# Performance work log

Measured on AMD Instinct MI355X. Metric: run time of the kernel, lower is better.

Reference implementation:

```python
import jax, jax.numpy as jnp
import numpy as np

B, F, D = 4096, 39, 16
L0, L1 = 128, 128
H1 = L0 // 2  # split_half: half the maps feed the next layer


def setup_inputs() -> dict:
    key = jax.random.key(0)
    k0, k1, k2, k3, k4 = jax.random.split(key, 5)
    x = jax.random.normal(k0, (B, F, D), dtype=jnp.float32)
    # Conv1D(size, 1, channels_first) == matmul over channel dim: W [out, in]
    W0 = jax.random.normal(k1, (L0, F * F), dtype=jnp.float32) * 0.02
    b0 = jnp.zeros((L0,), dtype=jnp.float32)
    W1 = jax.random.normal(k2, (L1, H1 * F), dtype=jnp.float32) * 0.02
    b1 = jnp.zeros((L1,), dtype=jnp.float32)
    return {"x": x, "W0": W0, "b0": b0, "W1": W1, "b1": b1}


def _cin_layer(h, h0, W, b):
    # h: [B, H, D], h0: [B, F, D] -> outer product [B, H*F, D], then 1x1 conv
    z = jnp.einsum('bhd,bmd->bhmd', h, h0)
    z = z.reshape(z.shape[0], -1, z.shape[-1])          # [B, H*F, D]
    y = jnp.einsum('oc,bcd->bod', W, z) + b[None, :, None]
    return jax.nn.relu(y)


def reference(x, W0, b0, W1, b1):
    h0 = x
    # layer 0 (split_half, not last): split into next_hidden / direct_connect
    y0 = _cin_layer(h0, h0, W0, b0)                     # [B, L0, D]
    next_hidden, direct0 = y0[:, :H1, :], y0[:, H1:, :]
    # layer 1 (last): all maps are direct connect
    direct1 = _cin_layer(next_hidden, h0, W1, b1)       # [B, L1, D]
    result = jnp.sum(jnp.concatenate([direct0, direct1], axis=1), axis=-1)
    return result  # [B, L0//2 + L1]
```

## Files before the change

kernel.cpp:

```cpp
#include <hip/hip_runtime.h>
#include <hip/hip_fp16.h>

#define B_     4096
#define F_     39
#define NKK    130
#define KKPAD  132
#define PFD    2
#define WPANEL ((size_t)KKPAD * 128)

typedef _Float16 f16x8  __attribute__((ext_vector_type(8)));
typedef float    f32x4  __attribute__((ext_vector_type(4)));
typedef float    f32x16 __attribute__((ext_vector_type(16)));

union FragAB { f16x8 h8; __half2 h2[4]; f32x4 f4; unsigned u[4]; __half h[8]; };

__global__ __launch_bounds__(256) void prep_w(
    const float* __restrict__ W0, const float* __restrict__ W1,
    __half* __restrict__ Wp)
{
    int idx = blockIdx.x * 256 + threadIdx.x;
    if (idx >= 4 * 130 * 1024) return;
    int j    = idx & 7;
    int lane = (idx >> 3) & 63;
    int ks   = (idx >> 9) & 1;
    int rest = idx >> 10;
    int kk   = rest % 130, Mt = rest / 130;
    int o    = Mt * 32 + (lane & 31);
    int sub  = lane >> 5;
    float v = 0.f;
    if (kk < 50) {
        int seg = kk / 10, kkin = kk - seg * 10;
        int h = 4 * kkin + 2 * ks + sub;
        int m = seg * 8 + j;
        if (h < 39 && m < 39) v = W0[o * 1521 + h * 39 + m];
    } else {
        int l = kk - 50;
        int seg = l / 10, kkin = l - seg * 10;
        int m = 4 * kkin + 2 * ks + sub;
        int h = seg * 8 + j;
        if (m < 39) v = W1[o * 2496 + h * 39 + m];
    }
    Wp[((size_t)(Mt * KKPAD + kk) * 2 + ks) * 512 + lane * 8 + j] = __float2half(v);
}

__global__ __launch_bounds__(256, 2) void cin_main(
    const float* __restrict__ x, const float* __restrict__ b0,
    const float* __restrict__ b1, const __half* __restrict__ Wp,
    float* __restrict__ out)
{
    __shared__ __align__(16) __half xT[8][16][40];
    __shared__ __align__(16) __half nhT[8][16][68];
    __shared__ float bs0[128], bs1[128];

    const int t    = threadIdx.x;
    const int w    = t >> 6, lane = t & 63;
    const int sub  = lane >> 5, bp = (lane >> 4) & 1, d = lane & 15;
    const int gb   = blockIdx.x * 8;

    const f32x4* Ap = (const f32x4*)Wp + (size_t)w * WPANEL + lane;
    FragAB An[PFD][2];
#pragma unroll
    for (int i = 0; i < PFD; ++i) {
        An[i][0].f4 = Ap[(size_t)i * 128];
        An[i][1].f4 = Ap[(size_t)i * 128 + 64];
    }

    if (t < 128) { bs0[t] = b0[t]; bs1[t] = b1[t]; }

    for (int i = t; i < 1248; i += 256) {
        int bt = i / 156, r2 = i - bt * 156;
        int f = r2 >> 2, dq = r2 & 3;
        float4 v = *(const float4*)&x[((size_t)(gb + bt) * F_ + f) * 16 + dq * 4];
        xT[bt][dq * 4 + 0][f] = __float2half(v.x);
        xT[bt][dq * 4 + 1][f] = __float2half(v.y);
        xT[bt][dq * 4 + 2][f] = __float2half(v.z);
        xT[bt][dq * 4 + 3][f] = __float2half(v.w);
    }
    if (t < 128) xT[t >> 4][t & 15][39] = __float2half(0.f);
    __syncthreads();

    FragAB xmc[4][5];
#pragma unroll
    for (int p = 0; p < 4; ++p)
#pragma unroll
        for (int a = 0; a < 5; ++a)
            xmc[p][a].f4 = *(const f32x4*)&xT[2 * p + bp][d][a * 8];

    const unsigned psel = sub ? 0x03020302u : 0x01000100u;

    f32x16 acc[4];
#pragma unroll
    for (int r = 0; r < 16; ++r) {
        float bv = bs0[w * 32 + (r & 3) + 8 * (r >> 2) + 4 * sub];
#pragma unroll
        for (int p = 0; p < 4; ++p) acc[p][r] = bv;
    }

    int kk = 0;
#pragma unroll 1
    for (int seg = 0; seg < 13; ++seg) {
        if (seg == 5) {
            if (w < 2) {
#pragma unroll
                for (int p = 0; p < 4; ++p) {
                    __half* nr = &nhT[2 * p + bp][d][0];
#pragma unroll
                    for (int rq = 0; rq < 4; ++rq) {
                        union { __half h[4]; float2 f2; } pk;
#pragma unroll
                        for (int q = 0; q < 4; ++q)
                            pk.h[q] = __float2half(fmaxf(acc[p][rq * 4 + q], 0.f));
                        *(float2*)(nr + w * 32 + 8 * rq + 4 * sub) = pk.f2;
                    }
                }
            } else {
#pragma unroll
                for (int p = 0; p < 4; ++p) {
#pragma unroll
                    for (int rq = 0; rq < 4; ++rq) {
                        float4 s; float* sv = (float*)&s;
#pragma unroll
                        for (int q = 0; q < 4; ++q) {
                            float v = fmaxf(acc[p][rq * 4 + q], 0.f);
                            v += __shfl_xor(v, 1); v += __shfl_xor(v, 2);
                            v += __shfl_xor(v, 4); v += __shfl_xor(v, 8);
                            sv[q] = v;
                        }
                        if (d == 0) {
                            int row = w * 32 + 8 * rq + 4 * sub;
                            *(float4*)&out[(size_t)(gb + 2 * p + bp) * 192 + (row - 64)] = s;
                        }
                    }
                }
            }
#pragma unroll
            for (int r = 0; r < 16; ++r) {
                float bv = bs1[w * 32 + (r & 3) + 8 * (r >> 2) + 4 * sub];
#pragma unroll
                for (int p = 0; p < 4; ++p) acc[p][r] = bv;
            }
            __syncthreads();
        }

        FragAB xcur[4];
        if (seg < 5) {
#pragma unroll
            for (int p = 0; p < 4; ++p)
                xcur[p].f4 = *(const f32x4*)&xT[2 * p + bp][d][seg * 8];
        } else {
#pragma unroll
            for (int p = 0; p < 4; ++p)
                xcur[p].f4 = *(const f32x4*)&nhT[2 * p + bp][d][(seg - 5) * 8];
        }

#pragma unroll
        for (int kkin = 0; kkin < 10; ++kkin) {
            const int s = kkin & 1;

            __builtin_amdgcn_s_setprio(1);
#pragma unroll
            for (int ks = 0; ks < 2; ++ks) {
                const int ee = 2 * kkin + ks;
#pragma unroll
                for (int p = 0; p < 4; ++p) {
                    unsigned bc = __builtin_amdgcn_perm(0u, xmc[p][ee >> 2].u[ee & 3], psel);
                    __half2 xh2 = *(__half2*)&bc;
                    FragAB bfr;
#pragma unroll
                    for (int q = 0; q < 4; ++q)
                        bfr.h2[q] = __hmul2(xcur[p].h2[q], xh2);
                    acc[p] = __builtin_amdgcn_mfma_f32_32x32x16_f16(
                        An[s][ks].h8, bfr.h8, acc[p], 0, 0, 0);
                }
            }
            __builtin_amdgcn_s_setprio(0);

            An[s][0].f4 = Ap[(size_t)(kk + PFD) * 128];
            An[s][1].f4 = Ap[(size_t)(kk + PFD) * 128 + 64];
            ++kk;
        }
    }

#pragma unroll
    for (int p = 0; p < 4; ++p) {
#pragma unroll
        for (int rq = 0; rq < 4; ++rq) {
            float4 s; float* sv = (float*)&s;
#pragma unroll
            for (int q = 0; q < 4; ++q) {
                float v = fmaxf(acc[p][rq * 4 + q], 0.f);
                v += __shfl_xor(v, 1); v += __shfl_xor(v, 2);
                v += __shfl_xor(v, 4); v += __shfl_xor(v, 8);
                sv[q] = v;
            }
            if (d == 0) {
                int row = w * 32 + 8 * rq + 4 * sub;
                *(float4*)&out[(size_t)(gb + 2 * p + bp) * 192 + 64 + row] = s;
            }
        }
    }
}

extern "C" void kernel_launch(void* const* d_in, const int* in_sizes, int n_in,
                              void* d_out, int out_size, void* d_ws, size_t ws_size,
                              hipStream_t stream) {
    const float* x  = (const float*)d_in[0];
    const float* W0 = (const float*)d_in[1];
    const float* b0 = (const float*)d_in[2];
    const float* W1 = (const float*)d_in[3];
    const float* b1 = (const float*)d_in[4];
    float* out = (float*)d_out;
    __half* Wp = (__half*)d_ws;

    prep_w<<<(4 * 130 * 1024 + 255) / 256, 256, 0, stream>>>(W0, W1, Wp);
    cin_main<<<B_ / 8, 256, 0, stream>>>(x, b0, b1, Wp, out);
}
```

Measured before the change: 74.12 us.

## Fully unroll segment loop with five-deep double-buffered weight fragment prefetch

Replaces the runtime segment loop with compile-time unrolled segment bodies that load weight A-fragments in batches of five k-steps into two register banks, alternating them so global loads overlap MFMA work. Layer-0 segments now read the x column straight from the resident xmc registers instead of reloading xT from LDS. The nhT row padding goes from 68 to 72 and the s_setprio hints are dropped. This trades many more VGPRs (20 fragment registers live) and larger code for deeper latency hiding, which risks spills or lower occupancy under the two-blocks-per-CU launch bound.

Measured after the change: 76.55 us. +3.3%, slower.

```diff
diff --git a/kernel.cpp b/kernel.cpp
--- a/kernel.cpp
+++ b/kernel.cpp
@@ -3,9 +3,7 @@
 
 #define B_     4096
 #define F_     39
-#define NKK    130
 #define KKPAD  132
-#define PFD    2
 #define WPANEL ((size_t)KKPAD * 128)
 
 typedef _Float16 f16x8  __attribute__((ext_vector_type(8)));
@@ -43,13 +41,66 @@
     Wp[((size_t)(Mt * KKPAD + kk) * 2 + ks) * 512 + lane * 8 + j] = __float2half(v);
 }
 
+template<int LL, int AA, int EB>
+__device__ __forceinline__ void compute_half(
+    const FragAB (&Areg)[5][2], const FragAB (&xmc)[4][5],
+    const FragAB (&xcur)[4], f32x16 (&acc)[4], unsigned psel)
+{
+#pragma unroll
+    for (int i = 0; i < 5; ++i) {
+#pragma unroll
+        for (int ks = 0; ks < 2; ++ks) {
+            const int ee = EB + 2 * i + ks;
+#pragma unroll
+            for (int p = 0; p < 4; ++p) {
+                unsigned bc = __builtin_amdgcn_perm(0u, xmc[p][ee >> 2].u[ee & 3], psel);
+                __half2 xh2 = *(__half2*)&bc;
+                FragAB bfr;
+#pragma unroll
+                for (int q = 0; q < 4; ++q) {
+                    if constexpr (LL == 0)
+                        bfr.h2[q] = __hmul2(xmc[p][AA].h2[q], xh2);
+                    else
+                        bfr.h2[q] = __hmul2(xcur[p].h2[q], xh2);
+                }
+                acc[p] = __builtin_amdgcn_mfma_f32_32x32x16_f16(
+                    Areg[i][ks].h8, bfr.h8, acc[p], 0, 0, 0);
+            }
+        }
+    }
+}
+
+template<int LL, int AA, bool LAST>
+__device__ __forceinline__ void seg_body(
+    const f32x4*& Apos,
+    FragAB (&Aa)[5][2], FragAB (&Ab)[5][2],
+    const FragAB (&xmc)[4][5], const FragAB (&xcur)[4],
+    f32x16 (&acc)[4], unsigned psel)
+{
+#pragma unroll
+    for (int i = 0; i < 5; ++i) {
+        Ab[i][0].f4 = Apos[(5 + i) * 128];
+        Ab[i][1].f4 = Apos[(5 + i) * 128 + 64];
+    }
+    compute_half<LL, AA, 0>(Aa, xmc, xcur, acc, psel);
+    if (!LAST) {
+#pragma unroll
+        for (int i = 0; i < 5; ++i) {
+            Aa[i][0].f4 = Apos[(10 + i) * 128];
+            Aa[i][1].f4 = Apos[(10 + i) * 128 + 64];
+        }
+    }
+    compute_half<LL, AA, 10>(Ab, xmc, xcur, acc, psel);
+    Apos += 1280;
+}
+
 __global__ __launch_bounds__(256, 2) void cin_main(
     const float* __restrict__ x, const float* __restrict__ b0,
     const float* __restrict__ b1, const __half* __restrict__ Wp,
     float* __restrict__ out)
 {
     __shared__ __align__(16) __half xT[8][16][40];
-    __shared__ __align__(16) __half nhT[8][16][68];
+    __shared__ __align__(16) __half nhT[8][16][72];
     __shared__ float bs0[128], bs1[128];
 
     const int t    = threadIdx.x;
@@ -57,12 +108,12 @@
     const int sub  = lane >> 5, bp = (lane >> 4) & 1, d = lane & 15;
     const int gb   = blockIdx.x * 8;
 
-    const f32x4* Ap = (const f32x4*)Wp + (size_t)w * WPANEL + lane;
-    FragAB An[PFD][2];
-#pragma unroll
-    for (int i = 0; i < PFD; ++i) {
-        An[i][0].f4 = Ap[(size_t)i * 128];
-        An[i][1].f4 = Ap[(size_t)i * 128 + 64];
+    const f32x4* Apos = (const f32x4*)Wp + (size_t)w * WPANEL + lane;
+    FragAB Aa[5][2], Ab[5][2];
+#pragma unroll
+    for (int i = 0; i < 5; ++i) {
+        Aa[i][0].f4 = Apos[i * 128];
+        Aa[i][1].f4 = Apos[i * 128 + 64];
     }
 
     if (t < 128) { bs0[t] = b0[t]; bs1[t] = b1[t]; }
@@ -96,90 +147,71 @@
         for (int p = 0; p < 4; ++p) acc[p][r] = bv;
     }
 
-    int kk = 0;
-#pragma unroll 1
-    for (int seg = 0; seg < 13; ++seg) {
-        if (seg == 5) {
-            if (w < 2) {
-#pragma unroll
-                for (int p = 0; p < 4; ++p) {
-                    __half* nr = &nhT[2 * p + bp][d][0];
-#pragma unroll
-                    for (int rq = 0; rq < 4; ++rq) {
-                        union { __half h[4]; float2 f2; } pk;
-#pragma unroll
-                        for (int q = 0; q < 4; ++q)
-                            pk.h[q] = __float2half(fmaxf(acc[p][rq * 4 + q], 0.f));
-                        *(float2*)(nr + w * 32 + 8 * rq + 4 * sub) = pk.f2;
-                    }
+    FragAB xcur[4];
+
+    seg_body<0, 0, false>(Apos, Aa, Ab, xmc, xcur, acc, psel);
+    seg_body<0, 1, false>(Apos, Aa, Ab, xmc, xcur, acc, psel);
+    seg_body<0, 2, false>(Apos, Aa, Ab, xmc, xcur, acc, psel);
+    seg_body<0, 3, false>(Apos, Aa, Ab, xmc, xcur, acc, psel);
+    seg_body<0, 4, false>(Apos, Aa, Ab, xmc, xcur, acc, psel);
+
+    if (w < 2) {
+#pragma unroll
+        for (int p = 0; p < 4; ++p) {
+            __half* nr = &nhT[2 * p + bp][d][0];
+#pragma unroll
+            for (int rq = 0; rq < 4; ++rq) {
+                union { __half h[4]; float2 f2; } pk;
+#pragma unroll
+                for (int q = 0; q < 4; ++q)
+                    pk.h[q] = __float2half(fmaxf(acc[p][rq * 4 + q], 0.f));
+                *(float2*)(nr + w * 32 + 8 * rq + 4 * sub) = pk.f2;
+            }
+        }
+    } else {
+#pragma unroll
+        for (int p = 0; p < 4; ++p) {
+#pragma unroll
+            for (int rq = 0; rq < 4; ++rq) {
+                float4 s; float* sv = (float*)&s;
+#pragma unroll
+                for (int q = 0; q < 4; ++q) {
+                    float v = fmaxf(acc[p][rq * 4 + q], 0.f);
+                    v += __shfl_xor(v, 1); v += __shfl_xor(v, 2);
+                    v += __shfl_xor(v, 4); v += __shfl_xor(v, 8);
+                    sv[q] = v;
                 }
-            } else {
-#pragma unroll
-                for (int p = 0; p < 4; ++p) {
-#pragma unroll
-                    for (int rq = 0; rq < 4; ++rq) {
-                        float4 s; float* sv = (float*)&s;
-#pragma unroll
-                        for (int q = 0; q < 4; ++q) {
-                            float v = fmaxf(acc[p][rq * 4 + q], 0.f);
-                            v += __shfl_xor(v, 1); v += __shfl_xor(v, 2);
-                            v += __shfl_xor(v, 4); v += __shfl_xor(v, 8);
-                            sv[q] = v;
-                        }
-                        if (d == 0) {
-                            int row = w * 32 + 8 * rq + 4 * sub;
-                            *(float4*)&out[(size_t)(gb + 2 * p + bp) * 192 + (row - 64)] = s;
-                        }
-                    }
+                if (d == 0) {
+                    int row = w * 32 + 8 * rq + 4 * sub;
+                    *(float4*)&out[(size_t)(gb + 2 * p + bp) * 192 + (row - 64)] = s;
                 }
             }
-#pragma unroll
-            for (int r = 0; r < 16; ++r) {
-                float bv = bs1[w * 32 + (r & 3) + 8 * (r >> 2) + 4 * sub];
-#pragma unroll
-                for (int p = 0; p < 4; ++p) acc[p][r] = bv;
-            }
-            __syncthreads();
-        }
-
-        FragAB xcur[4];
-        if (seg < 5) {
-#pragma unroll
-            for (int p = 0; p < 4; ++p)
-                xcur[p].f4 = *(const f32x4*)&xT[2 * p + bp][d][seg * 8];
-        } else {
-#pragma unroll
-            for (int p = 0; p < 4; ++p)
-                xcur[p].f4 = *(const f32x4*)&nhT[2 * p + bp][d][(seg - 5) * 8];
-        }
-
-#pragma unroll
-        for (int kkin = 0; kkin < 10; ++kkin) {
-            const int s = kkin & 1;
-
-            __builtin_amdgcn_s_setprio(1);
-#pragma unroll
-            for (int ks = 0; ks < 2; ++ks) {
-                const int ee = 2 * kkin + ks;
-#pragma unroll
-                for (int p = 0; p < 4; ++p) {
-                    unsigned bc = __builtin_amdgcn_perm(0u, xmc[p][ee >> 2].u[ee & 3], psel);
-                    __half2 xh2 = *(__half2*)&bc;
-                    FragAB bfr;
-#pragma unroll
-                    for (int q = 0; q < 4; ++q)
-                        bfr.h2[q] = __hmul2(xcur[p].h2[q], xh2);
-                    acc[p] = __builtin_amdgcn_mfma_f32_32x32x16_f16(
-                        An[s][ks].h8, bfr.h8, acc[p], 0, 0, 0);
-                }
-            }
-            __builtin_amdgcn_s_setprio(0);
-
-            An[s][0].f4 = Ap[(size_t)(kk + PFD) * 128];
-            An[s][1].f4 = Ap[(size_t)(kk + PFD) * 128 + 64];
-            ++kk;
-        }
-    }
+        }
+    }
+#pragma unroll
+    for (int r = 0; r < 16; ++r) {
+        float bv = bs1[w * 32 + (r & 3) + 8 * (r >> 2) + 4 * sub];
+#pragma unroll
+        for (int p = 0; p < 4; ++p) acc[p][r] = bv;
+    }
+    __syncthreads();
+
+#define L1_XCUR(AA_)                                                         \
+    {                                                                        \
+        xcur[0].f4 = *(const f32x4*)&nhT[bp][d][(AA_) * 8];                  \
+        xcur[1].f4 = *(const f32x4*)&nhT[2 + bp][d][(AA_) * 8];              \
+        xcur[2].f4 = *(const f32x4*)&nhT[4 + bp][d][(AA_) * 8];              \
+        xcur[3].f4 = *(const f32x4*)&nhT[6 + bp][d][(AA_) * 8];              \
+    }
+    L1_XCUR(0) seg_body<1, 0, false>(Apos, Aa, Ab, xmc, xcur, acc, psel);
+    L1_XCUR(1) seg_body<1, 1, false>(Apos, Aa, Ab, xmc, xcur, acc, psel);
+    L1_XCUR(2) seg_body<1, 2, false>(Apos, Aa, Ab, xmc, xcur, acc, psel);
+    L1_XCUR(3) seg_body<1, 3, false>(Apos, Aa, Ab, xmc, xcur, acc, psel);
+    L1_XCUR(4) seg_body<1, 4, false>(Apos, Aa, Ab, xmc, xcur, acc, psel);
+    L1_XCUR(5) seg_body<1, 5, false>(Apos, Aa, Ab, xmc, xcur, acc, psel);
+    L1_XCUR(6) seg_body<1, 6, false>(Apos, Aa, Ab, xmc, xcur, acc, psel);
+    L1_XCUR(7) seg_body<1, 7, true >(Apos, Aa, Ab, xmc, xcur, acc, psel);
+#undef L1_XCUR
 
 #pragma unroll
     for (int p = 0; p < 4; ++p) {
```

## Stream weight panels into LDS ring buffer via direct global-to-LDS loads

Applied to the files above, without the earlier changes.

Replaces the register double-buffered weight fragment prefetch with a 5-slot per-wave LDS ring filled by global_load_lds, three steps ahead, gated by explicit vmcnt waits. The segment loop is split into two phases so the layer-0 epilogue no longer sits inside the loop as a branch. This aims to deepen the prefetch and free VGPRs by keeping A operands in LDS. It costs LDS capacity (40KB for the ring), extra LDS reads per step, and depends on the hand-written vmcnt count being correct. It also drops the s_setprio hints.

After: 75.20 us. Within noise of the previous version (+1.5%).

```diff
diff --git a/kernel.cpp b/kernel.cpp
--- a/kernel.cpp
+++ b/kernel.cpp
@@ -1,18 +1,23 @@
 #include <hip/hip_runtime.h>
 #include <hip/hip_fp16.h>
+#include <stdint.h>
 
 #define B_     4096
 #define F_     39
-#define NKK    130
-#define KKPAD  132
-#define PFD    2
-#define WPANEL ((size_t)KKPAD * 128)
+#define KKPAD  133
+#define WPANEL ((size_t)KKPAD * 1024)
 
 typedef _Float16 f16x8  __attribute__((ext_vector_type(8)));
 typedef float    f32x4  __attribute__((ext_vector_type(4)));
 typedef float    f32x16 __attribute__((ext_vector_type(16)));
 
 union FragAB { f16x8 h8; __half2 h2[4]; f32x4 f4; unsigned u[4]; __half h[8]; };
+
+__device__ __forceinline__ void gload_lds16(const void* g, void* l) {
+    __builtin_amdgcn_global_load_lds(
+        (const __attribute__((address_space(1))) void*)g,
+        (__attribute__((address_space(3))) void*)l, 16, 0, 0);
+}
 
 __global__ __launch_bounds__(256) void prep_w(
     const float* __restrict__ W0, const float* __restrict__ W1,
@@ -40,7 +45,47 @@
         int h = seg * 8 + j;
         if (m < 39) v = W1[o * 2496 + h * 39 + m];
     }
-    Wp[((size_t)(Mt * KKPAD + kk) * 2 + ks) * 512 + lane * 8 + j] = __float2half(v);
+    Wp[(size_t)Mt * WPANEL + ((size_t)kk * 2 + ks) * 512 + lane * 8 + j] = __float2half(v);
+}
+
+__device__ __forceinline__ void inner10(
+    const __half* gpf, __half* As, int lane,
+    const FragAB (&xmc)[4][5], const FragAB (&xcur)[4],
+    f32x16 (&acc)[4], unsigned psel)
+{
+#pragma unroll
+    for (int kkin = 0; kkin < 10; ++kkin) {
+        const int slot = kkin % 5;
+
+        asm volatile("s_waitcnt vmcnt(4)" ::: "memory");
+
+        FragAB A0, A1;
+        A0.f4 = *(const f32x4*)(As + slot * 1024 + lane * 8);
+        A1.f4 = *(const f32x4*)(As + slot * 1024 + 512 + lane * 8);
+
+#pragma unroll
+        for (int ks = 0; ks < 2; ++ks) {
+            const int ee = 2 * kkin + ks;
+#pragma unroll
+            for (int p = 0; p < 4; ++p) {
+                unsigned bc = __builtin_amdgcn_perm(0u, xmc[p][ee >> 2].u[ee & 3], psel);
+                __half2 xh2 = *(__half2*)&bc;
+                FragAB bfr;
+#pragma unroll
+                for (int q = 0; q < 4; ++q)
+                    bfr.h2[q] = __hmul2(xcur[p].h2[q], xh2);
+                acc[p] = __builtin_amdgcn_mfma_f32_32x32x16_f16(
+                    (ks ? A1 : A0).h8, bfr.h8, acc[p], 0, 0, 0);
+            }
+        }
+
+        {
+            const __half* g = gpf + kkin * 1024 + lane * 8;
+            const int ws = ((kkin + 3) % 5) * 1024;
+            gload_lds16(g,       As + ws);
+            gload_lds16(g + 512, As + ws + 512);
+        }
+    }
 }
 
 __global__ __launch_bounds__(256, 2) void cin_main(
@@ -48,8 +93,9 @@
     const float* __restrict__ b1, const __half* __restrict__ Wp,
     float* __restrict__ out)
 {
+    __shared__ __align__(16) __half Asl[4][5][1024];
     __shared__ __align__(16) __half xT[8][16][40];
-    __shared__ __align__(16) __half nhT[8][16][68];
+    __shared__ __align__(16) __half nhT[8][16][72];
     __shared__ float bs0[128], bs1[128];
 
     const int t    = threadIdx.x;
@@ -57,12 +103,14 @@
     const int sub  = lane >> 5, bp = (lane >> 4) & 1, d = lane & 15;
     const int gb   = blockIdx.x * 8;
 
-    const f32x4* Ap = (const f32x4*)Wp + (size_t)w * WPANEL + lane;
-    FragAB An[PFD][2];
-#pragma unroll
-    for (int i = 0; i < PFD; ++i) {
-        An[i][0].f4 = Ap[(size_t)i * 128];
-        An[i][1].f4 = Ap[(size_t)i * 128 + 64];
+    __half* As = &Asl[w][0][0];
+    const __half* gp = Wp + (size_t)w * WPANEL;
+
+#pragma unroll
+    for (int k0 = 0; k0 < 3; ++k0) {
+        const __half* g = gp + (size_t)k0 * 1024 + lane * 8;
+        gload_lds16(g,       As + k0 * 1024);
+        gload_lds16(g + 512, As + k0 * 1024 + 512);
     }
 
     if (t < 128) { bs0[t] = b0[t]; bs1[t] = b1[t]; }
@@ -96,96 +144,73 @@
         for (int p = 0; p < 4; ++p) acc[p][r] = bv;
     }
 
-    int kk = 0;
+    const __half* gpf = gp + (size_t)3 * 1024;
 #pragma unroll 1
-    for (int seg = 0; seg < 13; ++seg) {
-        if (seg == 5) {
-            if (w < 2) {
-#pragma unroll
-                for (int p = 0; p < 4; ++p) {
-                    __half* nr = &nhT[2 * p + bp][d][0];
-#pragma unroll
-                    for (int rq = 0; rq < 4; ++rq) {
-                        union { __half h[4]; float2 f2; } pk;
-#pragma unroll
-                        for (int q = 0; q < 4; ++q)
-                            pk.h[q] = __float2half(fmaxf(acc[p][rq * 4 + q], 0.f));
-                        *(float2*)(nr + w * 32 + 8 * rq + 4 * sub) = pk.f2;
-                    }
+    for (int s = 0; s < 5; ++s) {
+        FragAB xcur[4];
+#pragma unroll
+        for (int p = 0; p < 4; ++p)
+            xcur[p].f4 = *(const f32x4*)(&xT[2 * p + bp][d][0] + s * 8);
+        inner10(gpf, As, lane, xmc, xcur, acc, psel);
+        gpf += 10 * 1024;
+    }
+
+    if (w < 2) {
+#pragma unroll
+        for (int p = 0; p < 4; ++p) {
+            __half* nr = &nhT[2 * p + bp][d][0];
+#pragma unroll
+            for (int rq = 0; rq < 4; ++rq) {
+                union { __half h[4]; float2 f2; } pk;
+#pragma unroll
+                for (int q = 0; q < 4; ++q)
+                    pk.h[q] = __float2half(fmaxf(acc[p][rq * 4 + q], 0.f));
+                *(float2*)(nr + w * 32 + 8 * rq + 4 * sub) = pk.f2;
+            }
+        }
+    } else {
+#pragma unroll
+        for (int p = 0; p < 4; ++p) {
+#pragma unroll
+            for (int rq = 0; rq < 4; ++rq) {
+                float4 s4; float* sv = (float*)&s4;
+#pragma unroll
+                for (int q = 0; q < 4; ++q) {
+                    float v = fmaxf(acc[p][rq * 4 + q], 0.f);
+                    v += __shfl_xor(v, 1); v += __shfl_xor(v, 2);
+                    v += __shfl_xor(v, 4); v += __shfl_xor(v, 8);
+                    sv[q] = v;
                 }
-            } else {
-#pragma unroll
-                for (int p = 0; p < 4; ++p) {
-#pragma unroll
-                    for (int rq = 0; rq < 4; ++rq) {
-                        float4 s; float* sv = (float*)&s;
-#pragma unroll
-                        for (int q = 0; q < 4; ++q) {
-                            float v = fmaxf(acc[p][rq * 4 + q], 0.f);
-                            v += __shfl_xor(v, 1); v += __shfl_xor(v, 2);
-                            v += __shfl_xor(v, 4); v += __shfl_xor(v, 8);
-                            sv[q] = v;
-                        }
-                        if (d == 0) {
-                            int row = w * 32 + 8 * rq + 4 * sub;
-                            *(float4*)&out[(size_t)(gb + 2 * p + bp) * 192 + (row - 64)] = s;
-                        }
-                    }
+                if (d == 0) {
+                    int row = w * 32 + 8 * rq + 4 * sub;
+                    *(float4*)&out[(size_t)(gb + 2 * p + bp) * 192 + (row - 64)] = s4;
                 }
             }
-#pragma unroll
-            for (int r = 0; r < 16; ++r) {
-                float bv = bs1[w * 32 + (r & 3) + 8 * (r >> 2) + 4 * sub];
-#pragma unroll
-                for (int p = 0; p < 4; ++p) acc[p][r] = bv;
-            }
-            __syncthreads();
-        }
-
+        }
+    }
+#pragma unroll
+    for (int r = 0; r < 16; ++r) {
+        float bv = bs1[w * 32 + (r & 3) + 8 * (r >> 2) + 4 * sub];
+#pragma unroll
+        for (int p = 0; p < 4; ++p) acc[p][r] = bv;
+    }
+    __syncthreads();
+
+#pragma unroll 1
+    for (int s = 0; s < 8; ++s) {
         FragAB xcur[4];
-        if (seg < 5) {
-#pragma unroll
-            for (int p = 0; p < 4; ++p)
-                xcur[p].f4 = *(const f32x4*)&xT[2 * p + bp][d][seg * 8];
-        } else {
-#pragma unroll
-            for (int p = 0; p < 4; ++p)
-                xcur[p].f4 = *(const f32x4*)&nhT[2 * p + bp][d][(seg - 5) * 8];
-        }
-
-#pragma unroll
-        for (int kkin = 0; kkin < 10; ++kkin) {
-            const int s = kkin & 1;
-
-            __builtin_amdgcn_s_setprio(1);
-#pragma unroll
-            for (int ks = 0; ks < 2; ++ks) {
-                const int ee = 2 * kkin + ks;
-#pragma unroll
-                for (int p = 0; p < 4; ++p) {
-                    unsigned bc = __builtin_amdgcn_perm(0u, xmc[p][ee >> 2].u[ee & 3], psel);
-                    __half2 xh2 = *(__half2*)&bc;
-                    FragAB bfr;
-#pragma unroll
-                    for (int q = 0; q < 4; ++q)
-                        bfr.h2[q] = __hmul2(xcur[p].h2[q], xh2);
-                    acc[p] = __builtin_amdgcn_mfma_f32_32x32x16_f16(
-                        An[s][ks].h8, bfr.h8, acc[p], 0, 0, 0);
-                }
-            }
-            __builtin_amdgcn_s_setprio(0);
-
-            An[s][0].f4 = Ap[(size_t)(kk + PFD) * 128];
-            An[s][1].f4 = Ap[(size_t)(kk + PFD) * 128 + 64];
-            ++kk;
-        }
+#pragma unroll
+        for (int p = 0; p < 4; ++p)
+            xcur[p].f4 = *(const f32x4*)(&nhT[2 * p + bp][d][0] + s * 8);
+        inner10(gpf, As, lane, xmc, xcur, acc, psel);
+        gpf += 10 * 1024;
     }
 
 #pragma unroll
     for (int p = 0; p < 4; ++p) {
 #pragma unroll
         for (int rq = 0; rq < 4; ++rq) {
-            float4 s; float* sv = (float*)&s;
+            float4 s4; float* sv = (float*)&s4;
 #pragma unroll
             for (int q = 0; q < 4; ++q) {
                 float v = fmaxf(acc[p][rq * 4 + q], 0.f);
@@ -195,7 +220,7 @@
             }
             if (d == 0) {
                 int row = w * 32 + 8 * rq + 4 * sub;
-                *(float4*)&out[(size_t)(gb + 2 * p + bp) * 192 + 64 + row] = s;
+                *(float4*)&out[(size_t)(gb + 2 * p + bp) * 192 + 64 + row] = s4;
             }
         }
     }
```
